# Optimization experiments

Hardware: AMD Instinct MI355X
Metric: run time of the kernel (lower is better)

Reference implementation:

```python
import jax, jax.numpy as jnp
import numpy as np

N = 50000      # nodes
E = 1600000    # edges (avg degree 32)
R = 8          # relation types
G = 64         # graphs in batch
D_IN = 128
HID = 128
CLS = 10


def setup_inputs() -> dict:
    key = jax.random.key(0)
    ks = jax.random.split(key, 12)
    s = 0.05  # weight init scale
    return {
        "x": jax.random.normal(ks[0], (N, D_IN), dtype=jnp.float32),
        "edge_index": jax.random.randint(ks[1], (2, E), 0, N, dtype=jnp.int32),
        "edge_type": jax.random.randint(ks[2], (E,), 0, R, dtype=jnp.int32),
        "batch": jnp.sort(jax.random.randint(ks[3], (N,), 0, G, dtype=jnp.int32)),
        "W1": jax.random.normal(ks[4], (R, D_IN, HID), dtype=jnp.float32) * s,
        "root1": jax.random.normal(ks[5], (D_IN, HID), dtype=jnp.float32) * s,
        "b1": jax.random.normal(ks[6], (HID,), dtype=jnp.float32) * s,
        "W2": jax.random.normal(ks[7], (R, HID, HID), dtype=jnp.float32) * s,
        "root2": jax.random.normal(ks[8], (HID, HID), dtype=jnp.float32) * s,
        "b2": jax.random.normal(ks[9], (HID,), dtype=jnp.float32) * s,
        "lin_w": jax.random.normal(ks[10], (HID, CLS), dtype=jnp.float32) * s,
        "lin_b": jax.random.normal(ks[11], (CLS,), dtype=jnp.float32) * s,
    }


def rgcn_conv(x, edge_index, edge_type, W, root, bias):
    # PyG RGCNConv (default aggr='mean'): per-relation mean of neighbor
    # features, relation-specific matmul, summed over relations, + root + bias.
    src, dst = edge_index[0], edge_index[1]
    d_in = x.shape[1]
    seg = dst * R + edge_type                      # fused (node, relation) segment id
    msg = jax.ops.segment_sum(x[src], seg, num_segments=N * R)          # [N*R, d_in]
    cnt = jax.ops.segment_sum(jnp.ones((E,), x.dtype), seg, num_segments=N * R)
    mean = (msg / jnp.maximum(cnt, 1.0)[:, None]).reshape(N, R, d_in)   # [N, R, d_in]
    return jnp.einsum('nrd,rdh->nh', mean, W) + x @ root + bias


def reference(x, edge_index, edge_type, batch, W1, root1, b1, W2, root2, b2, lin_w, lin_b):
    h = jax.nn.relu(rgcn_conv(x, edge_index, edge_type, W1, root1, b1))
    h = jax.nn.relu(rgcn_conv(h, edge_index, edge_type, W2, root2, b2))
    # global mean pool per graph
    gsum = jax.ops.segment_sum(h, batch, num_segments=G)                # [G, HID]
    gcnt = jax.ops.segment_sum(jnp.ones((N,), h.dtype), batch, num_segments=G)
    g = gsum / jnp.maximum(gcnt, 1.0)[:, None]
    return g @ lin_w + lin_b                                            # [G, CLS]
```

## Files before the change

### kernel.cpp

```cpp
#include <hip/hip_runtime.h>

#define N_NODES 50000
#define N_EDGES 1600000
#define R_REL 8
#define G_GRAPHS 64
#define D_INF 128
#define HIDF 128
#define CLSF 10

#define S_SEG (N_NODES * R_REL)
#define RZ 9
#define PCHUNK 16

#define XG 8
#define NODES_PER_G (N_NODES / XG)
#define SORT_BLKS_PER_G 256
#define SORT_GRID (XG * SORT_BLKS_PER_G)

typedef __attribute__((ext_vector_type(8))) short short8;
typedef __attribute__((ext_vector_type(4))) float floatx4;

typedef __attribute__((address_space(1))) const unsigned int guint;
typedef __attribute__((address_space(3))) unsigned int luint;
__device__ __forceinline__ void gload_lds16(const void* g, void* l) {
    __builtin_amdgcn_global_load_lds((guint*)g, (luint*)l, 16, 0, 0);
}

__device__ __forceinline__ unsigned short f2bf(float f) {
    unsigned int u = __float_as_uint(f);
    unsigned int r = (u + 0x7fffu + ((u >> 16) & 1u)) >> 16;
    return (unsigned short)r;
}
__device__ __forceinline__ float bflo(unsigned int u) { return __uint_as_float(u << 16); }
__device__ __forceinline__ float bfhi(unsigned int u) { return __uint_as_float(u & 0xffff0000u); }

__device__ __forceinline__ int ntload(const int* p) { return __builtin_nontemporal_load(p); }

__global__ void seg_kernel(const int* __restrict__ dst, const int* __restrict__ et,
                           int* __restrict__ seg) {
    int e = blockIdx.x * blockDim.x + threadIdx.x;
    if (e < N_EDGES) seg[e] = dst[e] * R_REL + et[e];
}

__global__ __launch_bounds__(256) void count_kernel(const int* __restrict__ seg,
                                                    int* __restrict__ cnt) {
    int xg = blockIdx.x & (XG - 1);
    int inner = blockIdx.x >> 3;
    int lo = xg * NODES_PER_G * R_REL, hi = lo + NODES_PER_G * R_REL;
    for (int e = inner * 256 + threadIdx.x; e < N_EDGES; e += SORT_BLKS_PER_G * 256) {
        int sg = ntload(seg + e);
        if (sg >= lo && sg < hi) atomicAdd(&cnt[sg], 1);
    }
}

#define SCAN_BLK 256
#define SCAN_ELEMS 1024
#define NB_SCAN ((S_SEG + SCAN_ELEMS - 1) / SCAN_ELEMS)

__global__ __launch_bounds__(SCAN_BLK) void scan1_kernel(const int* __restrict__ cnt,
                                                         int* __restrict__ off,
                                                         int* __restrict__ bsum) {
    __shared__ int sd[SCAN_BLK];
    int t = threadIdx.x;
    int base = blockIdx.x * SCAN_ELEMS + t * 4;
    int v[4];
    int tsum = 0;
#pragma unroll
    for (int j = 0; j < 4; j++) {
        v[j] = (base + j < S_SEG) ? cnt[base + j] : 0;
        tsum += v[j];
    }
    sd[t] = tsum;
    __syncthreads();
    for (int d = 1; d < SCAN_BLK; d <<= 1) {
        int x = (t >= d) ? sd[t - d] : 0;
        __syncthreads();
        sd[t] += x;
        __syncthreads();
    }
    int incl = sd[t];
    int run = incl - tsum;
#pragma unroll
    for (int j = 0; j < 4; j++) {
        if (base + j < S_SEG) off[base + j] = run;
        run += v[j];
    }
    if (t == SCAN_BLK - 1) bsum[blockIdx.x] = incl;
}

__global__ __launch_bounds__(512) void scan2_kernel(int* __restrict__ bsum) {
    __shared__ int sd[512];
    int t = threadIdx.x;
    int v = (t < NB_SCAN) ? bsum[t] : 0;
    sd[t] = v;
    __syncthreads();
    for (int d = 1; d < 512; d <<= 1) {
        int x = (t >= d) ? sd[t - d] : 0;
        __syncthreads();
        sd[t] += x;
        __syncthreads();
    }
    if (t < NB_SCAN) bsum[t] = sd[t] - v;
}

__global__ void absoff_kernel(int* __restrict__ off, const int* __restrict__ bsum,
                              const int* __restrict__ cnt, float* __restrict__ winv) {
    int i = blockIdx.x * blockDim.x + threadIdx.x;
    if (i < S_SEG) {
        off[i] += bsum[i >> 10];
        winv[i] = 1.0f / (float)max(cnt[i], 1);
    }
}

__global__ __launch_bounds__(256) void bin_kernel(const int* __restrict__ seg,
                                                  const int* __restrict__ src,
                                                  int* __restrict__ cursor,
                                                  int* __restrict__ esrc) {
    int xg = blockIdx.x & (XG - 1);
    int inner = blockIdx.x >> 3;
    int lo = xg * NODES_PER_G * R_REL, hi = lo + NODES_PER_G * R_REL;
    for (int e = inner * 256 + threadIdx.x; e < N_EDGES; e += SORT_BLKS_PER_G * 256) {
        int sg = ntload(seg + e);
        if (sg >= lo && sg < hi) {
            int pos = atomicAdd(&cursor[sg], 1);
            esrc[pos] = ntload(src + e);
        }
    }
}

__global__ void convx_kernel(const float* __restrict__ x, unsigned short* __restrict__ xb) {
    int idx = blockIdx.x * blockDim.x + threadIdx.x;
    if (idx < N_NODES * D_INF) xb[idx] = f2bf(x[idx]);
}

__global__ __launch_bounds__(256) void convw9_kernel(const float* __restrict__ W,
                                                     const float* __restrict__ root,
                                                     unsigned short* __restrict__ wz) {
    __shared__ float t[16][17];
    int r = blockIdx.z;
    int k0 = blockIdx.x * 16, c0 = blockIdx.y * 16;
    int tx = threadIdx.x & 15, ty = threadIdx.x >> 4;
    const float* srcp = (r < 8) ? (W + (size_t)r * 128 * 128) : root;
    t[ty][tx] = srcp[(size_t)(k0 + ty) * 128 + c0 + tx];
    __syncthreads();
    wz[(size_t)r * 16384 + (size_t)(c0 + ty) * 128 + k0 + tx] = f2bf(t[tx][ty]);
}

__global__ __launch_bounds__(256) void agg_mean(
    const unsigned short* __restrict__ hsrc,
    const int* __restrict__ esrc,
    const int* __restrict__ off,
    const float* __restrict__ winv,
    unsigned short* __restrict__ m)
{
    int sg = blockIdx.x * 16 + (threadIdx.x >> 4);
    int l = threadIdx.x & 15;
    int beg = off[sg];
    int end = (sg + 1 < S_SEG) ? off[sg + 1] : N_EDGES;
    float w = winv[sg];

    float a0 = 0.f, a1 = 0.f, a2 = 0.f, a3 = 0.f;
    float a4 = 0.f, a5 = 0.f, a6 = 0.f, a7 = 0.f;
    int e = beg;
    for (; e + 4 <= end; e += 4) {
        int s0 = esrc[e], s1 = esrc[e + 1], s2 = esrc[e + 2], s3 = esrc[e + 3];
        uint4 v0 = *(const uint4*)(hsrc + (size_t)s0 * HIDF + l * 8);
        uint4 v1 = *(const uint4*)(hsrc + (size_t)s1 * HIDF + l * 8);
        uint4 v2 = *(const uint4*)(hsrc + (size_t)s2 * HIDF + l * 8);
        uint4 v3 = *(const uint4*)(hsrc + (size_t)s3 * HIDF + l * 8);
        a0 += bflo(v0.x) + bflo(v1.x) + bflo(v2.x) + bflo(v3.x);
        a1 += bfhi(v0.x) + bfhi(v1.x) + bfhi(v2.x) + bfhi(v3.x);
        a2 += bflo(v0.y) + bflo(v1.y) + bflo(v2.y) + bflo(v3.y);
        a3 += bfhi(v0.y) + bfhi(v1.y) + bfhi(v2.y) + bfhi(v3.y);
        a4 += bflo(v0.z) + bflo(v1.z) + bflo(v2.z) + bflo(v3.z);
        a5 += bfhi(v0.z) + bfhi(v1.z) + bfhi(v2.z) + bfhi(v3.z);
        a6 += bflo(v0.w) + bflo(v1.w) + bflo(v2.w) + bflo(v3.w);
        a7 += bfhi(v0.w) + bfhi(v1.w) + bfhi(v2.w) + bfhi(v3.w);
    }
    for (; e < end; e++) {
        int s0 = esrc[e];
        uint4 v0 = *(const uint4*)(hsrc + (size_t)s0 * HIDF + l * 8);
        a0 += bflo(v0.x); a1 += bfhi(v0.x);
        a2 += bflo(v0.y); a3 += bfhi(v0.y);
        a4 += bflo(v0.z); a5 += bfhi(v0.z);
        a6 += bflo(v0.w); a7 += bfhi(v0.w);
    }
    uint4 o;
    o.x = (unsigned int)f2bf(a0 * w) | ((unsigned int)f2bf(a1 * w) << 16);
    o.y = (unsigned int)f2bf(a2 * w) | ((unsigned int)f2bf(a3 * w) << 16);
    o.z = (unsigned int)f2bf(a4 * w) | ((unsigned int)f2bf(a5 * w) << 16);
    o.w = (unsigned int)f2bf(a6 * w) | ((unsigned int)f2bf(a7 * w) << 16);
    *(uint4*)(m + (size_t)sg * HIDF + l * 8) = o;
}

__global__ __launch_bounds__(256) void transform9(
    const unsigned short* __restrict__ mm,
    const unsigned short* __restrict__ hsrc,
    const unsigned short* __restrict__ wz,
    const float* __restrict__ bias,
    unsigned short* __restrict__ hout)
{
    __shared__ __align__(16) unsigned short A4[4][128][32];
    __shared__ __align__(16) unsigned short B4[4][128][32];

    const int tx = threadIdx.x;
    const int wave = tx >> 6, lane = tx & 63;
    const int quad = lane >> 4, lq = lane & 15;
    const int srow = lane >> 2, sch = lane & 3;
    const int row0 = blockIdx.x * 128;

    floatx4 acc[2][8];
#pragma unroll
    for (int i = 0; i < 2; i++)
#pragma unroll
        for (int j = 0; j < 8; j++) acc[i][j] = (floatx4){0.f, 0.f, 0.f, 0.f};

    for (int r = 0; r < RZ; r++) {
#pragma unroll
        for (int kk = 0; kk < 4; kk++) {
#pragma unroll
            for (int p = 0; p < 2; p++) {
                int rr = (wave * 2 + p) * 16;
                int gr = row0 + rr + srow; if (gr >= N_NODES) gr = N_NODES - 1;
                const unsigned short* ap = (r < 8)
                    ? mm + (size_t)gr * (R_REL * HIDF) + r * HIDF
                    : hsrc + (size_t)gr * HIDF;
                gload_lds16(ap + kk * 32 + sch * 8, &A4[kk][rr][0]);
                gload_lds16(wz + ((size_t)r * 128 + rr + srow) * 128 + kk * 32 + sch * 8,
                            &B4[kk][rr][0]);
            }
        }
        __syncthreads();

#pragma unroll
        for (int kk = 0; kk < 4; kk++) {
            short8 af[2], bfr[8];
#pragma unroll
            for (int i = 0; i < 2; i++)
                af[i] = *(const short8*)(&A4[kk][wave * 32 + i * 16 + lq][quad * 8]);
#pragma unroll
            for (int j = 0; j < 8; j++)
                bfr[j] = *(const short8*)(&B4[kk][j * 16 + lq][quad * 8]);
#pragma unroll
            for (int i = 0; i < 2; i++)
#pragma unroll
                for (int j = 0; j < 8; j++)
                    acc[i][j] = __builtin_amdgcn_mfma_f32_16x16x32_bf16(af[i], bfr[j], acc[i][j], 0, 0, 0);
        }
        __syncthreads();
    }

#pragma unroll
    for (int i = 0; i < 2; i++)
#pragma unroll
        for (int j = 0; j < 8; j++) {
            int col = j * 16 + lq;
            float bv = bias[col];
#pragma unroll
            for (int rg = 0; rg < 4; rg++) {
                int row = row0 + wave * 32 + i * 16 + quad * 4 + rg;
                if (row < N_NODES)
                    hout[(size_t)row * HIDF + col] = f2bf(fmaxf(acc[i][j][rg] + bv, 0.f));
            }
        }
}

__global__ __launch_bounds__(256) void pool1_kernel(const unsigned short* __restrict__ h,
                                                    const int* __restrict__ batch,
                                                    float* __restrict__ partial) {
    int g = blockIdx.x;
    int p = blockIdx.y;
    int lo, hi;
    {
        int l = 0, r = N_NODES;
        while (l < r) { int m = (l + r) >> 1; if (batch[m] < g) l = m + 1; else r = m; }
        lo = l;
        l = lo; r = N_NODES;
        while (l < r) { int m = (l + r) >> 1; if (batch[m] < g + 1) l = m + 1; else r = m; }
        hi = l;
    }
    int t = threadIdx.x;
    int rowlane = t >> 5;
    int c4 = t & 31;
    float a0 = 0.f, a1 = 0.f, a2 = 0.f, a3 = 0.f;
    for (int n = lo + p + rowlane * PCHUNK; n < hi; n += 8 * PCHUNK) {
        uint2 v = *(const uint2*)(h + (size_t)n * HIDF + c4 * 4);
        a0 += bflo(v.x); a1 += bfhi(v.x); a2 += bflo(v.y); a3 += bfhi(v.y);
    }
    __shared__ float red[8][128];
    if (rowlane == 0) {
        red[0][c4 * 4 + 0] = a0; red[0][c4 * 4 + 1] = a1;
        red[0][c4 * 4 + 2] = a2; red[0][c4 * 4 + 3] = a3;
    }
    __syncthreads();
    for (int s = 1; s < 8; s++) {
        if (rowlane == s) {
            red[0][c4 * 4 + 0] += a0; red[0][c4 * 4 + 1] += a1;
            red[0][c4 * 4 + 2] += a2; red[0][c4 * 4 + 3] += a3;
        }
        __syncthreads();
    }
    if (t < 128) partial[((size_t)g * PCHUNK + p) * 128 + t] = red[0][t];
}

__global__ __launch_bounds__(128) void pool2_kernel(const float* __restrict__ partial,
                                                    const int* __restrict__ batch,
                                                    float* __restrict__ gmean) {
    int g = blockIdx.x;
    int lo, hi;
    {
        int l = 0, r = N_NODES;
        while (l < r) { int m = (l + r) >> 1; if (batch[m] < g) l = m + 1; else r = m; }
        lo = l;
        l = lo; r = N_NODES;
        while (l < r) { int m = (l + r) >> 1; if (batch[m] < g + 1) l = m + 1; else r = m; }
        hi = l;
    }
    int t = threadIdx.x;
    float s = 0.f;
#pragma unroll
    for (int p = 0; p < PCHUNK; p++)
        s += partial[((size_t)g * PCHUNK + p) * 128 + t];
    gmean[g * HIDF + t] = s / (float)max(hi - lo, 1);
}

__global__ void final_kernel(const float* __restrict__ gmean,
                             const float* __restrict__ lin_w,
                             const float* __restrict__ lin_b,
                             float* __restrict__ out) {
    __shared__ float gl[HIDF];
    int g = blockIdx.x;
    int hh = threadIdx.x;
    gl[hh] = gmean[g * HIDF + hh];
    __syncthreads();
    if (hh < CLSF) {
        float s = lin_b[hh];
#pragma unroll 16
        for (int d = 0; d < HIDF; d++) s += gl[d] * lin_w[d * CLSF + hh];
        out[g * CLSF + hh] = s;
    }
}

extern "C" void kernel_launch(void* const* d_in, const int* in_sizes, int n_in,
                              void* d_out, int out_size, void* d_ws, size_t ws_size,
                              hipStream_t stream) {
    const float* x     = (const float*)d_in[0];
    const int*   ei    = (const int*)d_in[1];
    const int*   et    = (const int*)d_in[2];
    const int*   batch = (const int*)d_in[3];
    const float* W1    = (const float*)d_in[4];
    const float* root1 = (const float*)d_in[5];
    const float* b1    = (const float*)d_in[6];
    const float* W2    = (const float*)d_in[7];
    const float* root2 = (const float*)d_in[8];
    const float* b2    = (const float*)d_in[9];
    const float* lin_w = (const float*)d_in[10];
    const float* lin_b = (const float*)d_in[11];
    float* out = (float*)d_out;

    const int* src = ei;
    const int* dst = ei + N_EDGES;

    char* ws = (char*)d_ws;
    unsigned short* xb  = (unsigned short*)ws; ws += (size_t)N_NODES * HIDF * 2;
    unsigned short* h1  = (unsigned short*)ws; ws += (size_t)N_NODES * HIDF * 2;
    unsigned short* h2  = (unsigned short*)ws; ws += (size_t)N_NODES * HIDF * 2;
    unsigned short* m   = (unsigned short*)ws; ws += (size_t)S_SEG * HIDF * 2;
    unsigned short* wz1 = (unsigned short*)ws; ws += (size_t)RZ * 128 * 128 * 2;
    unsigned short* wz2 = (unsigned short*)ws; ws += (size_t)RZ * 128 * 128 * 2;
    int*   seg    = (int*)ws;   ws += (size_t)N_EDGES * 4;
    int*   cnt    = (int*)ws;   ws += (size_t)S_SEG * 4;
    int*   off    = (int*)ws;   ws += (size_t)S_SEG * 4;
    int*   bsum   = (int*)ws;   ws += 512 * 4;
    int*   cursor = (int*)ws;   ws += (size_t)S_SEG * 4;
    float* winv   = (float*)ws; ws += (size_t)S_SEG * 4;
    int*   esrc   = (int*)ws;   ws += (size_t)N_EDGES * 4;
    float* partial = (float*)ws; ws += (size_t)G_GRAPHS * PCHUNK * 128 * 4;
    float* gmean  = (float*)ws; ws += (size_t)G_GRAPHS * HIDF * 4;

    hipMemsetAsync(cnt, 0, (size_t)S_SEG * 4, stream);

    seg_kernel<<<(N_EDGES + 255) / 256, 256, 0, stream>>>(dst, et, seg);
    count_kernel<<<SORT_GRID, 256, 0, stream>>>(seg, cnt);
    scan1_kernel<<<NB_SCAN, SCAN_BLK, 0, stream>>>(cnt, off, bsum);
    scan2_kernel<<<1, 512, 0, stream>>>(bsum);
    absoff_kernel<<<(S_SEG + 255) / 256, 256, 0, stream>>>(off, bsum, cnt, winv);
    hipMemcpyAsync(cursor, off, (size_t)S_SEG * 4, hipMemcpyDeviceToDevice, stream);
    bin_kernel<<<SORT_GRID, 256, 0, stream>>>(seg, src, cursor, esrc);

    convx_kernel<<<(N_NODES * D_INF + 255) / 256, 256, 0, stream>>>(x, xb);
    convw9_kernel<<<dim3(8, 8, RZ), 256, 0, stream>>>(W1, root1, wz1);
    convw9_kernel<<<dim3(8, 8, RZ), 256, 0, stream>>>(W2, root2, wz2);

    const int NGB = (N_NODES + 127) / 128;
    const int NSB = S_SEG / 16;

    agg_mean<<<NSB, 256, 0, stream>>>(xb, esrc, off, winv, m);
    transform9<<<NGB, 256, 0, stream>>>(m, xb, wz1, b1, h1);

    agg_mean<<<NSB, 256, 0, stream>>>(h1, esrc, off, winv, m);
    transform9<<<NGB, 256, 0, stream>>>(m, h1, wz2, b2, h2);

    pool1_kernel<<<dim3(G_GRAPHS, PCHUNK), 256, 0, stream>>>(h2, batch, partial);
    pool2_kernel<<<G_GRAPHS, 128, 0, stream>>>(partial, batch, gmean);
    final_kernel<<<G_GRAPHS, HIDF, 0, stream>>>(gmean, lin_w, lin_b, out);

    (void)in_sizes; (void)n_in; (void)out_size; (void)ws_size;
}
```

Before: 473.6 us.

## Fuse scan/offset and pooling kernels, narrow edge source indices to 16-bit

Merges the second-level scan, absolute-offset fixup and cursor copy into one kernel where each block rescans the block sums, and fuses the pooling finish with the final linear layer. Edge source indices are stored as 16-bit values, halving index traffic in the aggregation passes, and the mean weight is computed from segment bounds instead of a precomputed array. The segment kernel is vectorised to int4. This removes several launches and memory round trips but relies on node ids fitting in 16 bits.

```diff
diff --git a/kernel.cpp b/kernel.cpp
--- a/kernel.cpp
+++ b/kernel.cpp
@@ -36,10 +36,17 @@
 
 __device__ __forceinline__ int ntload(const int* p) { return __builtin_nontemporal_load(p); }
 
-__global__ void seg_kernel(const int* __restrict__ dst, const int* __restrict__ et,
-                           int* __restrict__ seg) {
-    int e = blockIdx.x * blockDim.x + threadIdx.x;
-    if (e < N_EDGES) seg[e] = dst[e] * R_REL + et[e];
+__global__ __launch_bounds__(256) void seg_kernel(const int* __restrict__ dst,
+                                                  const int* __restrict__ et,
+                                                  int* __restrict__ seg) {
+    int i4 = blockIdx.x * 256 + threadIdx.x;
+    if (i4 * 4 >= N_EDGES) return;
+    int4 d = ((const int4*)dst)[i4];
+    int4 t = ((const int4*)et)[i4];
+    int4 s;
+    s.x = d.x * R_REL + t.x; s.y = d.y * R_REL + t.y;
+    s.z = d.z * R_REL + t.z; s.w = d.w * R_REL + t.w;
+    ((int4*)seg)[i4] = s;
 }
 
 __global__ __launch_bounds__(256) void count_kernel(const int* __restrict__ seg,
@@ -88,7 +95,9 @@
     if (t == SCAN_BLK - 1) bsum[blockIdx.x] = incl;
 }
 
-__global__ __launch_bounds__(512) void scan2_kernel(int* __restrict__ bsum) {
+__global__ __launch_bounds__(512) void absoff2_kernel(int* __restrict__ off,
+                                                      const int* __restrict__ bsum,
+                                                      int* __restrict__ cursor) {
     __shared__ int sd[512];
     int t = threadIdx.x;
     int v = (t < NB_SCAN) ? bsum[t] : 0;
@@ -100,22 +109,23 @@
         sd[t] += x;
         __syncthreads();
     }
-    if (t < NB_SCAN) bsum[t] = sd[t] - v;
-}
-
-__global__ void absoff_kernel(int* __restrict__ off, const int* __restrict__ bsum,
-                              const int* __restrict__ cnt, float* __restrict__ winv) {
-    int i = blockIdx.x * blockDim.x + threadIdx.x;
-    if (i < S_SEG) {
-        off[i] += bsum[i >> 10];
-        winv[i] = 1.0f / (float)max(cnt[i], 1);
+    int pre = (blockIdx.x == 0) ? 0 : sd[blockIdx.x - 1];
+    int base = blockIdx.x * SCAN_ELEMS + t * 2;
+#pragma unroll
+    for (int j = 0; j < 2; j++) {
+        int i = base + j;
+        if (i < S_SEG) {
+            int o = off[i] + pre;
+            off[i] = o;
+            cursor[i] = o;
+        }
     }
 }
 
 __global__ __launch_bounds__(256) void bin_kernel(const int* __restrict__ seg,
                                                   const int* __restrict__ src,
                                                   int* __restrict__ cursor,
-                                                  int* __restrict__ esrc) {
+                                                  unsigned short* __restrict__ esrc) {
     int xg = blockIdx.x & (XG - 1);
     int inner = blockIdx.x >> 3;
     int lo = xg * NODES_PER_G * R_REL, hi = lo + NODES_PER_G * R_REL;
@@ -123,7 +133,7 @@
         int sg = ntload(seg + e);
         if (sg >= lo && sg < hi) {
             int pos = atomicAdd(&cursor[sg], 1);
-            esrc[pos] = ntload(src + e);
+            esrc[pos] = (unsigned short)ntload(src + e);
         }
     }
 }
@@ -148,16 +158,15 @@
 
 __global__ __launch_bounds__(256) void agg_mean(
     const unsigned short* __restrict__ hsrc,
-    const int* __restrict__ esrc,
+    const unsigned short* __restrict__ esrc,
     const int* __restrict__ off,
-    const float* __restrict__ winv,
     unsigned short* __restrict__ m)
 {
     int sg = blockIdx.x * 16 + (threadIdx.x >> 4);
     int l = threadIdx.x & 15;
     int beg = off[sg];
     int end = (sg + 1 < S_SEG) ? off[sg + 1] : N_EDGES;
-    float w = winv[sg];
+    float w = 1.0f / (float)max(end - beg, 1);
 
     float a0 = 0.f, a1 = 0.f, a2 = 0.f, a3 = 0.f;
     float a4 = 0.f, a5 = 0.f, a6 = 0.f, a7 = 0.f;
@@ -303,9 +312,12 @@
     if (t < 128) partial[((size_t)g * PCHUNK + p) * 128 + t] = red[0][t];
 }
 
-__global__ __launch_bounds__(128) void pool2_kernel(const float* __restrict__ partial,
-                                                    const int* __restrict__ batch,
-                                                    float* __restrict__ gmean) {
+__global__ __launch_bounds__(128) void poolfin_kernel(const float* __restrict__ partial,
+                                                      const int* __restrict__ batch,
+                                                      const float* __restrict__ lin_w,
+                                                      const float* __restrict__ lin_b,
+                                                      float* __restrict__ out) {
+    __shared__ float gl[HIDF];
     int g = blockIdx.x;
     int lo, hi;
     {
@@ -321,23 +333,13 @@
 #pragma unroll
     for (int p = 0; p < PCHUNK; p++)
         s += partial[((size_t)g * PCHUNK + p) * 128 + t];
-    gmean[g * HIDF + t] = s / (float)max(hi - lo, 1);
-}
-
-__global__ void final_kernel(const float* __restrict__ gmean,
-                             const float* __restrict__ lin_w,
-                             const float* __restrict__ lin_b,
-                             float* __restrict__ out) {
-    __shared__ float gl[HIDF];
-    int g = blockIdx.x;
-    int hh = threadIdx.x;
-    gl[hh] = gmean[g * HIDF + hh];
+    gl[t] = s / (float)max(hi - lo, 1);
     __syncthreads();
-    if (hh < CLSF) {
-        float s = lin_b[hh];
+    if (t < CLSF) {
+        float acc = lin_b[t];
 #pragma unroll 16
-        for (int d = 0; d < HIDF; d++) s += gl[d] * lin_w[d * CLSF + hh];
-        out[g * CLSF + hh] = s;
+        for (int d = 0; d < HIDF; d++) acc += gl[d] * lin_w[d * CLSF + t];
+        out[g * CLSF + t] = acc;
     }
 }
 
@@ -373,19 +375,15 @@
     int*   off    = (int*)ws;   ws += (size_t)S_SEG * 4;
     int*   bsum   = (int*)ws;   ws += 512 * 4;
     int*   cursor = (int*)ws;   ws += (size_t)S_SEG * 4;
-    float* winv   = (float*)ws; ws += (size_t)S_SEG * 4;
-    int*   esrc   = (int*)ws;   ws += (size_t)N_EDGES * 4;
+    unsigned short* esrc = (unsigned short*)ws; ws += (size_t)N_EDGES * 2;
     float* partial = (float*)ws; ws += (size_t)G_GRAPHS * PCHUNK * 128 * 4;
-    float* gmean  = (float*)ws; ws += (size_t)G_GRAPHS * HIDF * 4;
 
     hipMemsetAsync(cnt, 0, (size_t)S_SEG * 4, stream);
 
-    seg_kernel<<<(N_EDGES + 255) / 256, 256, 0, stream>>>(dst, et, seg);
+    seg_kernel<<<(N_EDGES / 4 + 255) / 256, 256, 0, stream>>>(dst, et, seg);
     count_kernel<<<SORT_GRID, 256, 0, stream>>>(seg, cnt);
     scan1_kernel<<<NB_SCAN, SCAN_BLK, 0, stream>>>(cnt, off, bsum);
-    scan2_kernel<<<1, 512, 0, stream>>>(bsum);
-    absoff_kernel<<<(S_SEG + 255) / 256, 256, 0, stream>>>(off, bsum, cnt, winv);
-    hipMemcpyAsync(cursor, off, (size_t)S_SEG * 4, hipMemcpyDeviceToDevice, stream);
+    absoff2_kernel<<<NB_SCAN, 512, 0, stream>>>(off, bsum, cursor);
     bin_kernel<<<SORT_GRID, 256, 0, stream>>>(seg, src, cursor, esrc);
 
     convx_kernel<<<(N_NODES * D_INF + 255) / 256, 256, 0, stream>>>(x, xb);
@@ -395,15 +393,14 @@
     const int NGB = (N_NODES + 127) / 128;
     const int NSB = S_SEG / 16;
 
-    agg_mean<<<NSB, 256, 0, stream>>>(xb, esrc, off, winv, m);
+    agg_mean<<<NSB, 256, 0, stream>>>(xb, esrc, off, m);
     transform9<<<NGB, 256, 0, stream>>>(m, xb, wz1, b1, h1);
 
-    agg_mean<<<NSB, 256, 0, stream>>>(h1, esrc, off, winv, m);
+    agg_mean<<<NSB, 256, 0, stream>>>(h1, esrc, off, m);
     transform9<<<NGB, 256, 0, stream>>>(m, h1, wz2, b2, h2);
 
     pool1_kernel<<<dim3(G_GRAPHS, PCHUNK), 256, 0, stream>>>(h2, batch, partial);
-    pool2_kernel<<<G_GRAPHS, 128, 0, stream>>>(partial, batch, gmean);
-    final_kernel<<<G_GRAPHS, HIDF, 0, stream>>>(gmean, lin_w, lin_b, out);
+    poolfin_kernel<<<G_GRAPHS, 128, 0, stream>>>(partial, batch, lin_w, lin_b, out);
 
     (void)in_sizes; (void)n_in; (void)out_size; (void)ws_size;
 }
```

Result: faster. 461.7 us (-2.5%).
